# Kernel optimization log

Measured on AMD Instinct MI355X. Metric: run time of the kernel, lower is better.

Reference implementation:

```python
import jax, jax.numpy as jnp
import numpy as np

B, C, H, W = 8, 80, 128, 128
K = 100
MAX_OBJS = 128
N_GT = 256  # 32 GT boxes per image
HM_W, WH_W, OFF_W = 1.0, 0.1, 1.0
BETA = 0.1  # iou_map weight ('Ct IoU Loss x 0.1')


def setup_inputs() -> dict:
    key = jax.random.key(0)
    ks = jax.random.split(key, 12)
    hm = jax.random.normal(ks[0], (B, C, H, W), jnp.float32)
    wh = jax.random.normal(ks[1], (B, 2, H, W), jnp.float32) * 2.0 + 8.0
    reg = jax.random.normal(ks[2], (B, 2, H, W), jnp.float32) * 0.1
    hm_target = jax.random.uniform(ks[3], (B, C, H, W), jnp.float32) * 0.99
    wh_target = jax.random.uniform(ks[4], (B, MAX_OBJS, 2), jnp.float32) * 20.0 + 2.0
    reg_target = jax.random.uniform(ks[5], (B, MAX_OBJS, 2), jnp.float32)
    reg_mask = jax.random.randint(ks[6], (B, MAX_OBJS), 0, 2).astype(jnp.int32)
    ind = jax.random.randint(ks[7], (B, MAX_OBJS), 0, H * W).astype(jnp.int32)
    cx = jax.random.uniform(ks[8], (N_GT,)) * (W - 1)
    cy = jax.random.uniform(ks[9], (N_GT,)) * (H - 1)
    bw = jax.random.uniform(ks[10], (N_GT,)) * 30.0 + 2.0
    bh = jax.random.uniform(ks[11], (N_GT,)) * 30.0 + 2.0
    target_box = jnp.stack([cx - bw / 2, cy - bh / 2, cx + bw / 2, cy + bh / 2], -1).astype(jnp.float32)
    target_bidx = jnp.repeat(jnp.arange(B), N_GT // B).astype(jnp.int32)
    return {"hm": hm, "wh": wh, "reg": reg, "hm_target": hm_target,
            "wh_target": wh_target, "reg_target": reg_target,
            "reg_mask": reg_mask, "ind": ind,
            "target_box": target_box, "target_bidx": target_bidx}


def _gather_feat(feat, ind):
    # feat [B, ch, H, W], ind [B, M] spatial indices -> [B, M, ch]
    b, ch = feat.shape[0], feat.shape[1]
    f = feat.reshape(b, ch, -1).transpose(0, 2, 1)  # [B, HW, ch]
    return jnp.take_along_axis(f, ind[:, :, None], axis=1)


def _pairwise_iou(boxes1, boxes2):
    # boxes1 [K,4], boxes2 [N,4], xyxy -> [K,N]
    a1 = jnp.maximum(boxes1[:, 2] - boxes1[:, 0], 0.0) * jnp.maximum(boxes1[:, 3] - boxes1[:, 1], 0.0)
    a2 = jnp.maximum(boxes2[:, 2] - boxes2[:, 0], 0.0) * jnp.maximum(boxes2[:, 3] - boxes2[:, 1], 0.0)
    lt = jnp.maximum(boxes1[:, None, :2], boxes2[None, :, :2])
    rb = jnp.minimum(boxes1[:, None, 2:], boxes2[None, :, 2:])
    whi = jnp.clip(rb - lt, 0.0)
    inter = whi[..., 0] * whi[..., 1]
    union = a1[:, None] + a2[None, :] - inter
    return inter / jnp.maximum(union, 1e-7)


def _decode(hm_s, wh, reg):
    # _nms: 3x3 max-pool peak keeping
    hmax = jax.lax.reduce_window(hm_s, -jnp.inf, jax.lax.max,
                                 (1, 1, 3, 3), (1, 1, 1, 1),
                                 [(0, 0), (0, 0), (1, 1), (1, 1)])
    hm_k = jnp.where(hmax == hm_s, hm_s, 0.0)
    # global top-K over C*H*W (equivalent to per-class topK then topK-of-topK)
    scores, inds = jax.lax.top_k(hm_k.reshape(B, -1), K)
    clses = inds // (H * W)
    sinds = inds % (H * W)
    ys_i = sinds // W
    xs_i = sinds % W
    r = _gather_feat(reg, sinds)  # [B,K,2] sub-pixel offsets
    xs = xs_i.astype(jnp.float32) + r[..., 0]
    ys = ys_i.astype(jnp.float32) + r[..., 1]
    w = _gather_feat(wh, sinds)   # [B,K,2]
    boxes = jnp.stack([xs - w[..., 0] / 2, ys - w[..., 1] / 2,
                       xs + w[..., 0] / 2, ys + w[..., 1] / 2], -1)
    return boxes, scores, clses, ys_i, xs_i


def _focal_loss(pred, gt):
    # CenterNet focal loss; pred already sigmoid+clamped
    pos = gt == 1.0
    neg_w = (1.0 - gt) ** 4
    pos_loss = jnp.sum(jnp.where(pos, jnp.log(pred) * (1.0 - pred) ** 2, 0.0))
    neg_loss = jnp.sum(jnp.where(pos, 0.0, jnp.log(1.0 - pred) * pred ** 2 * neg_w))
    num_pos = jnp.sum(pos.astype(jnp.float32))
    return jnp.where(num_pos > 0, -(pos_loss + neg_loss) / jnp.maximum(num_pos, 1.0), -neg_loss)


def _reg_l1(out, mask, ind, tgt):
    pred = _gather_feat(out, ind)                       # [B, M, 2]
    m = jnp.broadcast_to(mask.astype(jnp.float32)[:, :, None], pred.shape)
    return jnp.sum(jnp.abs(pred * m - tgt * m)) / (jnp.sum(m) + 1e-4)


def reference(hm, wh, reg, hm_target, wh_target, reg_target, reg_mask, ind, target_box, target_bidx):
    hm_s = jnp.clip(jax.nn.sigmoid(hm), 1e-4, 1.0 - 1e-4)  # _sigmoid
    boxes, scores, clses, ys_i, xs_i = _decode(hm_s, wh, reg)
    # per-image pairwise IoU vs GT boxes of the same image, max over GT
    iou_all = jax.vmap(lambda bx: _pairwise_iou(bx, target_box))(boxes)  # [B,K,N]
    bmask = target_bidx[None, None, :] == jnp.arange(B)[:, None, None]
    iou = jnp.max(jnp.where(bmask, iou_all, 0.0), axis=-1)              # [B,K]
    # scatter IoU into dense heatmap-shaped iou_map at (b, cls, y, x)
    b_idx = jnp.broadcast_to(jnp.arange(B)[:, None], (B, K))
    iou_map = jnp.zeros_like(hm_s).at[b_idx, clses, ys_i, xs_i].set(iou)
    hm_t = jnp.clip(hm_target + BETA * iou_map, 0.0, 1.0)
    hm_loss = _focal_loss(hm_s, hm_t)
    wh_loss = _reg_l1(wh, reg_mask, ind, wh_target)
    off_loss = _reg_l1(reg, reg_mask, ind, reg_target)
    loss = HM_W * hm_loss + WH_W * wh_loss + OFF_W * off_loss
    return loss, hm_loss, wh_loss, off_loss
```

## Files before the change

kernel.cpp:

```cpp
#include <hip/hip_runtime.h>
#include <math.h>

#define B_ 8
#define C_ 80
#define H_ 128
#define W_ 128
#define K_ 100
#define MAXOBJS_ 128
#define NGT_ 256
#define HW_ (H_*W_)
#define CHW_ (C_*H_*W_)
#define TOT_ (B_*CHW_)
#define NBINS_ 4096
#define BCAP_ 4096
#define DCAP_ 128
#define CAPLDS_ 3072
#define DLOC_ 128
#define BLOC_ 768
#define NEGINF_ (-INFINITY)

#define OFF_LISTCNT 96
#define OFF_HIST   128
#define OFF_THR    131200
#define OFF_CNTA   131264
#define OFF_CNTB   131296
#define OFF_DEFV   131328
#define OFF_DEFI   135424
#define OFF_BORV   139520
#define OFF_BORI   270592
#define OFF_LIST   401664
#define ZERO_BYTES 131328
#define CAP_REQ    196608ull
#define CAP_MAX    262144ull

__device__ __forceinline__ unsigned skey(float x){
    unsigned u = __float_as_uint(x);
    return (u & 0x80000000u) ? ~u : (u | 0x80000000u);
}

__device__ __forceinline__ void find_thr(const unsigned* __restrict__ lh,
                                         unsigned* __restrict__ part,
                                         unsigned target,
                                         unsigned* out_thr, unsigned* out_cum){
    int t = threadIdx.x;
    unsigned s = 0;
    #pragma unroll
    for(int k=0;k<16;++k) s += lh[t*16+k];
    part[t] = s;
    __syncthreads();
    for(int off=1; off<256; off<<=1){
        unsigned v = (t+off<256) ? part[t+off] : 0u;
        __syncthreads();
        part[t] += v;
        __syncthreads();
    }
    unsigned nxt = (t<255) ? part[t+1] : 0u;
    if(part[t] >= target && nxt < target){
        unsigned cum = nxt;
        int thr = t*16;
        for(int bin=t*16+15; bin>=t*16; --bin){
            unsigned c = lh[bin];
            if(cum + c >= target){ thr = bin; break; }
            cum += c;
        }
        *out_thr = (unsigned)thr;
        *out_cum = cum;
    }
    __syncthreads();
}

struct Row { float v[4]; float le, re; };

__device__ __forceinline__ Row loadrow(const float* __restrict__ P, int y, int xq){
    Row r;
    if(y < 0 || y >= H_){
        r.v[0]=r.v[1]=r.v[2]=r.v[3]=r.le=r.re=NEGINF_;
        return r;
    }
    const float4 f = *(const float4*)(P + y*W_ + xq*4);
    r.v[0]=f.x; r.v[1]=f.y; r.v[2]=f.z; r.v[3]=f.w;
    r.le = (xq==0) ? NEGINF_ : P[y*W_ + xq*4 - 1];
    r.re = (xq==31)? NEGINF_ : P[y*W_ + xq*4 + 4];
    return r;
}

__device__ __forceinline__ void hmax4(const Row& r, float h[4]){
    h[0]=fmaxf(fmaxf(r.le,  r.v[0]), r.v[1]);
    h[1]=fmaxf(fmaxf(r.v[0],r.v[1]), r.v[2]);
    h[2]=fmaxf(fmaxf(r.v[1],r.v[2]), r.v[3]);
    h[3]=fmaxf(fmaxf(r.v[2],r.v[3]), r.re);
}

__global__ __launch_bounds__(256) void k_main(const float* __restrict__ hm,
        const float* __restrict__ hmt, unsigned* __restrict__ hist,
        double* __restrict__ accum, unsigned* __restrict__ listcnt,
        int2* __restrict__ list, int capB){
    __shared__ unsigned lh[NBINS_];
    __shared__ int2 lbuf[CAPLDS_];
    __shared__ unsigned lcnt, lbase;
    __shared__ float red[256];
    int t = threadIdx.x;
    int plane = blockIdx.x;
    int b = plane / C_;
    int cls = plane - b*C_;
    const float* P = hm  + (size_t)plane*HW_;
    const float* T = hmt + (size_t)plane*HW_;
    int idx0 = cls*HW_;

    for(int i=t;i<NBINS_;i+=256) lh[i]=0u;
    if(t==0) lcnt=0u;
    __syncthreads();

    int xq = t & 31;
    int y0 = (t >> 5) * 16;
    Row rp = loadrow(P, y0-1, xq);
    Row rc = loadrow(P, y0,   xq);
    float hp[4], hc[4];
    hmax4(rp, hp); hmax4(rc, hc);
    float acc = 0.f;
    for(int rr=0; rr<16; ++rr){
        int y = y0 + rr;
        Row rn = loadrow(P, y+1, xq);
        float hn[4]; hmax4(rn, hn);
        float lr[4];
        lr[0]=fmaxf(rc.le,  rc.v[1]);
        lr[1]=fmaxf(rc.v[0],rc.v[2]);
        lr[2]=fmaxf(rc.v[1],rc.v[3]);
        lr[3]=fmaxf(rc.v[2],rc.re);
        float4 tg = *(const float4*)(T + y*W_ + xq*4);
        float tgv[4] = {tg.x, tg.y, tg.z, tg.w};
        #pragma unroll
        for(int j=0;j<4;++j){
            float v = rc.v[j];
            bool pk = (v>=lr[j]) && (v>=hp[j]) && (v>=hn[j]);
            if(pk){
                atomicAdd(&lh[skey(v)>>20], 1u);
                if(capB){
                    unsigned p = atomicAdd(&lcnt, 1u);
                    int2 e; e.x = __float_as_int(v); e.y = idx0 + y*W_ + xq*4 + j;
                    if(p < CAPLDS_) lbuf[p] = e;
                    else {
                        unsigned g = atomicAdd(&listcnt[b], 1u);
                        if(g < (unsigned)capB) list[(size_t)b*capB + g] = e;
                    }
                }
            }
            float pr = 1.f/(1.f + __expf(-v));
            pr = fminf(fmaxf(pr, 1e-4f), 1.f - 1e-4f);
            float q = 1.f - tgv[j]; float q2 = q*q;
            acc += __logf(1.f - pr) * pr * pr * q2 * q2;
        }
        rc = rn;
        #pragma unroll
        for(int j=0;j<4;++j){ hp[j]=hc[j]; hc[j]=hn[j]; }
    }
    __syncthreads();
    unsigned n = lcnt; if(n > CAPLDS_) n = CAPLDS_;
    if(capB && t==0) lbase = atomicAdd(&listcnt[b], n);
    for(int i=t;i<NBINS_;i+=256){ unsigned c=lh[i]; if(c) atomicAdd(&hist[b*NBINS_+i], c); }
    red[t] = acc;
    __syncthreads();
    if(capB){
        for(unsigned i=t;i<n;i+=256){
            unsigned g = lbase + i;
            if(g < (unsigned)capB) list[(size_t)b*capB + g] = lbuf[i];
        }
    }
    for(int s=128;s>0;s>>=1){
        if(t<s) red[t]+=red[t+s];
        __syncthreads();
    }
    if(t==0) atomicAdd(&accum[0], (double)red[0]);
}

__global__ __launch_bounds__(256) void k_scan(const int2* __restrict__ list,
        const unsigned* __restrict__ listcnt, int capB,
        const unsigned* __restrict__ hist,
        unsigned* __restrict__ cntA, unsigned* __restrict__ cntB,
        float* __restrict__ defv, int* __restrict__ defi,
        float* __restrict__ borv, int* __restrict__ bori){
    __shared__ unsigned lh[NBINS_];
    __shared__ unsigned part[256];
    __shared__ unsigned thrs, cums;
    __shared__ int2 dloc[DLOC_];
    __shared__ int2 bloc[BLOC_];
    __shared__ unsigned dc, bc, dbase, bbase;
    int b = blockIdx.x >> 6;
    int chunk = blockIdx.x & 63;
    int t = threadIdx.x;
    for(int i=t;i<NBINS_;i+=256) lh[i]=hist[b*NBINS_+i];
    if(t==0){ dc=0u; bc=0u; thrs=0u; cums=0u; }
    __syncthreads();
    find_thr(lh, part, (unsigned)K_, &thrs, &cums);
    unsigned thr = thrs;
    unsigned n = listcnt[b]; if(n > (unsigned)capB) n = (unsigned)capB;
    for(unsigned i = chunk*256u + t; i < n; i += 64u*256u){
        int2 e = list[(size_t)b*capB + i];
        float v = __int_as_float(e.x);
        unsigned bin = skey(v) >> 20;
        if(bin > thr){
            unsigned p = atomicAdd(&dc, 1u);
            if(p < DLOC_) dloc[p] = e;
            else { unsigned g = atomicAdd(&cntA[b],1u); if(g<DCAP_){ defv[b*DCAP_+g]=v; defi[b*DCAP_+g]=e.y; } }
        } else if(bin == thr){
            unsigned p = atomicAdd(&bc, 1u);
            if(p < BLOC_) bloc[p] = e;
            else { unsigned g = atomicAdd(&cntB[b],1u); if(g<BCAP_){ borv[b*BCAP_+g]=v; bori[b*BCAP_+g]=e.y; } }
        }
    }
    __syncthreads();
    unsigned dn = dc < DLOC_ ? dc : DLOC_;
    unsigned bn = bc < BLOC_ ? bc : BLOC_;
    if(t==0){
        dbase = dn ? atomicAdd(&cntA[b], dn) : 0u;
        bbase = bn ? atomicAdd(&cntB[b], bn) : 0u;
    }
    __syncthreads();
    for(unsigned i=t;i<dn;i+=256){
        unsigned g = dbase + i;
        if(g < DCAP_){ defv[b*DCAP_+g]=__int_as_float(dloc[i].x); defi[b*DCAP_+g]=dloc[i].y; }
    }
    for(unsigned i=t;i<bn;i+=256){
        unsigned g = bbase + i;
        if(g < BCAP_){ borv[b*BCAP_+g]=__int_as_float(bloc[i].x); bori[b*BCAP_+g]=bloc[i].y; }
    }
}

__global__ void k_thresh(const unsigned* __restrict__ hist, unsigned* __restrict__ thrbin){
    __shared__ unsigned lh[NBINS_];
    __shared__ unsigned part[256];
    __shared__ unsigned thrs, cums;
    int b = blockIdx.x, t = threadIdx.x;
    for(int i=t;i<NBINS_;i+=256) lh[i]=hist[b*NBINS_+i];
    if(t==0){ thrs=0u; cums=0u; }
    __syncthreads();
    find_thr(lh, part, (unsigned)K_, &thrs, &cums);
    if(t==0) thrbin[b]=thrs;
}

__device__ __forceinline__ bool is_peak_scalar(const float* __restrict__ hm, int idx, float v){
    int w = idx & (W_-1);
    int h = (idx >> 7) & (H_-1);
    bool peak = true;
    #pragma unroll
    for(int dy=-1; dy<=1; ++dy){
        int hh = h + dy;
        if(hh < 0 || hh >= H_) continue;
        #pragma unroll
        for(int dx=-1; dx<=1; ++dx){
            if(dy==0 && dx==0) continue;
            int ww = w + dx;
            if(ww < 0 || ww >= W_) continue;
            peak = peak && (v >= __ldg(&hm[idx + dy*W_ + dx]));
        }
    }
    return peak;
}

__global__ __launch_bounds__(256) void k_collect(const float* __restrict__ hm,
        const unsigned* __restrict__ thrbin,
        unsigned* __restrict__ cntA, unsigned* __restrict__ cntB,
        float* __restrict__ defv, int* __restrict__ defi,
        float* __restrict__ borv, int* __restrict__ bori){
    int idx = blockIdx.x*256 + threadIdx.x;
    float v = hm[idx];
    if(!is_peak_scalar(hm, idx, v)) return;
    int b = idx / CHW_;
    unsigned bin = skey(v) >> 20;
    unsigned thr = thrbin[b];
    if(bin > thr){
        unsigned p = atomicAdd(&cntA[b], 1u);
        if(p < DCAP_){ defv[b*DCAP_+p] = v; defi[b*DCAP_+p] = idx - b*CHW_; }
    } else if(bin == thr){
        unsigned p = atomicAdd(&cntB[b], 1u);
        if(p < BCAP_){ borv[b*BCAP_+p] = v; bori[b*BCAP_+p] = idx - b*CHW_; }
    }
}

__global__ __launch_bounds__(256) void k_select(const float* __restrict__ hm,
        const float* __restrict__ hmt, const float* __restrict__ wh,
        const float* __restrict__ reg, const float* __restrict__ tbox,
        const int* __restrict__ tbid,
        const unsigned* __restrict__ cntA, const unsigned* __restrict__ cntB,
        const float* __restrict__ defv, const int* __restrict__ defi,
        const float* __restrict__ borv, const int* __restrict__ bori,
        double* __restrict__ accum, int* __restrict__ misc){
    int b = blockIdx.x, t = threadIdx.x;
    __shared__ float sbox[NGT_][4];
    __shared__ int   sbid[NGT_];
    __shared__ float sv[BCAP_];
    __shared__ int   si[BCAP_];
    __shared__ unsigned h2[NBINS_];
    __shared__ unsigned t4[BCAP_];
    __shared__ unsigned part[256];
    __shared__ int  rvI[256];
    __shared__ int  sel[K_];
    __shared__ unsigned selc, t3c, t4c;
    __shared__ unsigned thr2s, cum2s, thr3s, need3s;
    __shared__ int wsel;

    int nA = (int)cntA[b]; if(nA>DCAP_) nA=DCAP_; if(nA>K_) nA=K_;
    int nB = (int)cntB[b]; if(nB>BCAP_) nB=BCAP_;
    int m = K_ - nA; if(m>nB) m=nB; if(m<0) m=0;

    for(int i=t;i<NGT_;i+=256){
        sbox[i][0]=tbox[i*4+0]; sbox[i][1]=tbox[i*4+1];
        sbox[i][2]=tbox[i*4+2]; sbox[i][3]=tbox[i*4+3];
        sbid[i]=tbid[i];
    }
    for(int i=t;i<nB;i+=256){ sv[i]=borv[b*BCAP_+i]; si[i]=bori[b*BCAP_+i]; }
    for(int i=t;i<nA;i+=256) sel[i]=defi[b*DCAP_+i];
    if(t==0){ selc=(unsigned)nA; t3c=0u; t4c=0u; thr2s=0u; cum2s=0u; thr3s=0u; need3s=0u; }
    for(int i=t;i<NBINS_;i+=256) h2[i]=0u;
    __syncthreads();

    if(m>0){
        for(int i=t;i<nB;i+=256) atomicAdd(&h2[(skey(sv[i])>>8)&0xFFFu], 1u);
        __syncthreads();
        find_thr(h2, part, (unsigned)m, &thr2s, &cum2s);
        unsigned thr2 = thr2s, need2 = (unsigned)m - cum2s;
        for(int i=t;i<nB;i+=256){
            unsigned sb=(skey(sv[i])>>8)&0xFFFu;
            if(sb>thr2){ unsigned p=atomicAdd(&selc,1u); if(p<K_) sel[p]=si[i]; }
            else if(sb==thr2){ unsigned p=atomicAdd(&t3c,1u); if(p<BCAP_) t4[p]=(unsigned)i; }
        }
        __syncthreads();
        unsigned nt3=t3c; if(nt3>BCAP_) nt3=BCAP_;
        part[t]=0u;
        __syncthreads();
        for(unsigned i=t;i<nt3;i+=256) atomicAdd(&part[skey(sv[t4[i]])&0xFFu], 1u);
        __syncthreads();
        for(int off=1; off<256; off<<=1){
            unsigned v = (t+off<256)? part[t+off] : 0u;
            __syncthreads();
            part[t] += v;
            __syncthreads();
        }
        {
            unsigned nxt = (t<255)? part[t+1] : 0u;
            if(part[t] >= need2 && nxt < need2){ thr3s=(unsigned)t; need3s=need2-nxt; }
        }
        __syncthreads();
        unsigned thr3=thr3s, need3=need3s;
        for(unsigned i=t;i<nt3;i+=256){
            unsigned ci=t4[i];
            unsigned lb=skey(sv[ci])&0xFFu;
            if(lb>thr3){ unsigned p=atomicAdd(&selc,1u); if(p<K_) sel[p]=si[ci]; }
            else if(lb==thr3){ unsigned p=atomicAdd(&t4c,1u); if(p<NBINS_) h2[p]=(unsigned)si[ci]; }
        }
        __syncthreads();
        unsigned n4=t4c; if(n4>NBINS_) n4=NBINS_;
        if(need3 >= n4){
            for(unsigned i=t;i<n4;i+=256){ unsigned p=atomicAdd(&selc,1u); if(p<K_) sel[p]=(int)h2[i]; }
            __syncthreads();
        } else {
            for(unsigned it=0; it<need3; ++it){
                int bi=0x7FFFFFFF;
                for(unsigned i=t;i<n4;i+=256){ int w=(int)h2[i]; bi = (w<bi)?w:bi; }
                rvI[t]=bi;
                __syncthreads();
                for(int st=128;st>0;st>>=1){
                    if(t<st){ int w=rvI[t+st]; if(w<rvI[t]) rvI[t]=w; }
                    __syncthreads();
                }
                if(t==0){ wsel=rvI[0]; unsigned p=selc; selc=p+1u; if(p<K_) sel[p]=wsel; }
                __syncthreads();
                int w=wsel;
                for(unsigned i=t;i<n4;i+=256) if((int)h2[i]==w) h2[i]=0x7FFFFFFFu;
                __syncthreads();
            }
        }
    }
    __syncthreads();

    int nsel=(int)selc; if(nsel>K_) nsel=K_;
    for(int k=t;k<nsel;k+=256){
        int idx = sel[k];
        int cls = idx / HW_;
        int sp  = idx - cls*HW_;
        int yi  = sp >> 7;
        int xi  = sp & (W_-1);
        float r0 = reg[(b*2+0)*HW_ + sp];
        float r1 = reg[(b*2+1)*HW_ + sp];
        float w0 = wh[(b*2+0)*HW_ + sp];
        float w1 = wh[(b*2+1)*HW_ + sp];
        float xs = (float)xi + r0;
        float ys = (float)yi + r1;
        float x1 = xs - w0*0.5f, y1 = ys - w1*0.5f;
        float x2 = xs + w0*0.5f, y2 = ys + w1*0.5f;
        float a1 = fmaxf(x2-x1, 0.f) * fmaxf(y2-y1, 0.f);
        float best = 0.f;
        for(int g=0; g<NGT_; ++g){
            if(sbid[g] != b) continue;
            float gx1=sbox[g][0], gy1=sbox[g][1], gx2=sbox[g][2], gy2=sbox[g][3];
            float a2 = fmaxf(gx2-gx1, 0.f) * fmaxf(gy2-gy1, 0.f);
            float ix1 = fmaxf(x1,gx1), iy1 = fmaxf(y1,gy1);
            float ix2 = fminf(x2,gx2), iy2 = fminf(y2,gy2);
            float iw = fmaxf(ix2-ix1, 0.f), ih = fmaxf(iy2-iy1, 0.f);
            float inter = iw*ih;
            float uni = a1 + a2 - inter;
            float iou = inter / fmaxf(uni, 1e-7f);
            best = fmaxf(best, iou);
        }
        int gidx = b*CHW_ + idx;
        float v = hm[gidx];
        float p = 1.f/(1.f + __expf(-v));
        p = fminf(fmaxf(p, 1e-4f), 1.f - 1e-4f);
        float gt0 = hmt[gidx];
        float q0 = 1.f - gt0; float q02 = q0*q0;
        float neg0 = __logf(1.f - p) * p * p * q02 * q02;
        float gt1 = fminf(gt0 + 0.1f*best, 1.f);
        if(gt1 == 1.f){
            atomicAdd(&misc[0], 1);
            float op = 1.f - p;
            atomicAdd(&accum[1], (double)(__logf(p)*op*op));
            atomicAdd(&accum[2], (double)(-neg0));
        } else {
            float q1 = 1.f - gt1; float q12 = q1*q1;
            float neg1 = __logf(1.f - p) * p * p * q12 * q12;
            atomicAdd(&accum[2], (double)(neg1 - neg0));
        }
    }
}

__global__ void k_regfinal(const float* __restrict__ wh, const float* __restrict__ reg,
        const float* __restrict__ wht, const float* __restrict__ regt,
        const int* __restrict__ mask, const int* __restrict__ ind,
        const double* __restrict__ accum, const int* __restrict__ misc,
        float* __restrict__ out){
    int tid = threadIdx.x;
    float whn = 0.f, offn = 0.f, ms = 0.f;
    for(int i=tid; i<B_*MAXOBJS_; i+=256){
        int b = i / MAXOBJS_;
        float mk = (float)mask[i];
        int id = ind[i];
        float p0 = wh[(b*2+0)*HW_ + id], p1 = wh[(b*2+1)*HW_ + id];
        whn += mk*(fabsf(p0 - wht[2*i]) + fabsf(p1 - wht[2*i+1]));
        float q0 = reg[(b*2+0)*HW_ + id], q1 = reg[(b*2+1)*HW_ + id];
        offn += mk*(fabsf(q0 - regt[2*i]) + fabsf(q1 - regt[2*i+1]));
        ms += 2.f*mk;
    }
    __shared__ float r0[256], r1[256], r2[256];
    r0[tid]=whn; r1[tid]=offn; r2[tid]=ms;
    __syncthreads();
    for(int st=128; st>0; st>>=1){
        if(tid<st){ r0[tid]+=r0[tid+st]; r1[tid]+=r1[tid+st]; r2[tid]+=r2[tid+st]; }
        __syncthreads();
    }
    if(tid==0){
        double neg = accum[0] + accum[2];
        double pos = accum[1];
        int np = misc[0];
        float hm_loss;
        if(np > 0) hm_loss = (float)(-(pos + neg) / (double)(np < 1 ? 1 : np));
        else       hm_loss = (float)(-neg);
        float msum = r2[0];
        float wh_loss  = r0[0] / (msum + 1e-4f);
        float off_loss = r1[0] / (msum + 1e-4f);
        float loss = hm_loss + 0.1f*wh_loss + off_loss;
        out[0]=loss; out[1]=hm_loss; out[2]=wh_loss; out[3]=off_loss;
    }
}

extern "C" void kernel_launch(void* const* d_in, const int* in_sizes, int n_in,
                              void* d_out, int out_size, void* d_ws, size_t ws_size,
                              hipStream_t stream){
    const float* hm   = (const float*)d_in[0];
    const float* wh   = (const float*)d_in[1];
    const float* reg  = (const float*)d_in[2];
    const float* hmt  = (const float*)d_in[3];
    const float* wht  = (const float*)d_in[4];
    const float* regt = (const float*)d_in[5];
    const int*   mask = (const int*)d_in[6];
    const int*   ind  = (const int*)d_in[7];
    const float* tbox = (const float*)d_in[8];
    const int*   tbid = (const int*)d_in[9];

    char* ws = (char*)d_ws;
    double*   accum   = (double*)ws;
    int*      misc    = (int*)(ws + 64);
    unsigned* listcnt = (unsigned*)(ws + OFF_LISTCNT);
    unsigned* hist    = (unsigned*)(ws + OFF_HIST);
    unsigned* thrbin  = (unsigned*)(ws + OFF_THR);
    unsigned* cntA    = (unsigned*)(ws + OFF_CNTA);
    unsigned* cntB    = (unsigned*)(ws + OFF_CNTB);
    float*    defv    = (float*)(ws + OFF_DEFV);
    int*      defi    = (int*)(ws + OFF_DEFI);
    float*    borv    = (float*)(ws + OFF_BORV);
    int*      bori    = (int*)(ws + OFF_BORI);
    int2*     list    = (int2*)(ws + OFF_LIST);

    size_t capB = 0;
    if(ws_size >= (size_t)OFF_LIST + CAP_REQ*(size_t)B_*8ull){
        capB = (ws_size - (size_t)OFF_LIST) / ((size_t)B_*8ull);
        if(capB > CAP_MAX) capB = CAP_MAX;
    }

    hipMemsetAsync(ws, 0, ZERO_BYTES, stream);
    k_main<<<B_*C_, 256, 0, stream>>>(hm, hmt, hist, accum, listcnt, list, (int)capB);
    if(capB){
        k_scan<<<B_*64, 256, 0, stream>>>(list, listcnt, (int)capB, hist,
                                          cntA, cntB, defv, defi, borv, bori);
    } else {
        k_thresh<<<B_, 256, 0, stream>>>(hist, thrbin);
        k_collect<<<TOT_/256, 256, 0, stream>>>(hm, thrbin, cntA, cntB,
                                                defv, defi, borv, bori);
    }
    k_select<<<B_, 256, 0, stream>>>(hm, hmt, wh, reg, tbox, tbid, cntA, cntB,
                                     defv, defi, borv, bori, accum, misc);
    k_regfinal<<<1, 256, 0, stream>>>(wh, reg, wht, regt, mask, ind, accum, misc,
                                      (float*)d_out);
    (void)in_sizes; (void)n_in; (void)out_size;
}
```

Baseline: 95.97 us.

## Split heatmap planes across two blocks, aggregate list appends per wavefront, hoist threshold

```diff
diff --git a/kernel.cpp b/kernel.cpp
--- a/kernel.cpp
+++ b/kernel.cpp
@@ -14,7 +14,7 @@
 #define NBINS_ 4096
 #define BCAP_ 4096
 #define DCAP_ 128
-#define CAPLDS_ 3072
+#define CAPLDS_ 1536
 #define DLOC_ 128
 #define BLOC_ 768
 #define NEGINF_ (-INFINITY)
@@ -100,25 +100,27 @@
     __shared__ unsigned lcnt, lbase;
     __shared__ float red[256];
     int t = threadIdx.x;
-    int plane = blockIdx.x;
+    int plane = blockIdx.x >> 1;
+    int half  = blockIdx.x & 1;
     int b = plane / C_;
     int cls = plane - b*C_;
     const float* P = hm  + (size_t)plane*HW_;
     const float* T = hmt + (size_t)plane*HW_;
     int idx0 = cls*HW_;
+    unsigned lane = (unsigned)(t & 63);
 
     for(int i=t;i<NBINS_;i+=256) lh[i]=0u;
     if(t==0) lcnt=0u;
     __syncthreads();
 
     int xq = t & 31;
-    int y0 = (t >> 5) * 16;
+    int y0 = half*64 + (t >> 5) * 8;
     Row rp = loadrow(P, y0-1, xq);
     Row rc = loadrow(P, y0,   xq);
     float hp[4], hc[4];
     hmax4(rp, hp); hmax4(rc, hc);
     float acc = 0.f;
-    for(int rr=0; rr<16; ++rr){
+    for(int rr=0; rr<8; ++rr){
         int y = y0 + rr;
         Row rn = loadrow(P, y+1, xq);
         float hn[4]; hmax4(rn, hn);
@@ -133,10 +135,18 @@
         for(int j=0;j<4;++j){
             float v = rc.v[j];
             bool pk = (v>=lr[j]) && (v>=hp[j]) && (v>=hn[j]);
-            if(pk){
-                atomicAdd(&lh[skey(v)>>20], 1u);
-                if(capB){
-                    unsigned p = atomicAdd(&lcnt, 1u);
+            if(pk) atomicAdd(&lh[skey(v)>>20], 1u);
+            if(capB){
+                unsigned long long mask = __ballot(pk);
+                int cnt = __popcll(mask);
+                unsigned pre = (unsigned)__popcll(mask & ((1ull<<lane)-1ull));
+                int base = 0;
+                if(cnt){
+                    if(lane==0) base = (int)atomicAdd(&lcnt, (unsigned)cnt);
+                    base = __shfl(base, 0, 64);
+                }
+                if(pk){
+                    unsigned p = (unsigned)base + pre;
                     int2 e; e.x = __float_as_int(v); e.y = idx0 + y*W_ + xq*4 + j;
                     if(p < CAPLDS_) lbuf[p] = e;
                     else {
@@ -173,26 +183,33 @@
     if(t==0) atomicAdd(&accum[0], (double)red[0]);
 }
 
+__global__ void k_thresh(const unsigned* __restrict__ hist, unsigned* __restrict__ thrbin){
+    __shared__ unsigned lh[NBINS_];
+    __shared__ unsigned part[256];
+    __shared__ unsigned thrs, cums;
+    int b = blockIdx.x, t = threadIdx.x;
+    for(int i=t;i<NBINS_;i+=256) lh[i]=hist[b*NBINS_+i];
+    if(t==0){ thrs=0u; cums=0u; }
+    __syncthreads();
+    find_thr(lh, part, (unsigned)K_, &thrs, &cums);
+    if(t==0) thrbin[b]=thrs;
+}
+
 __global__ __launch_bounds__(256) void k_scan(const int2* __restrict__ list,
         const unsigned* __restrict__ listcnt, int capB,
-        const unsigned* __restrict__ hist,
+        const unsigned* __restrict__ thrbin,
         unsigned* __restrict__ cntA, unsigned* __restrict__ cntB,
         float* __restrict__ defv, int* __restrict__ defi,
         float* __restrict__ borv, int* __restrict__ bori){
-    __shared__ unsigned lh[NBINS_];
-    __shared__ unsigned part[256];
-    __shared__ unsigned thrs, cums;
     __shared__ int2 dloc[DLOC_];
     __shared__ int2 bloc[BLOC_];
     __shared__ unsigned dc, bc, dbase, bbase;
     int b = blockIdx.x >> 6;
     int chunk = blockIdx.x & 63;
     int t = threadIdx.x;
-    for(int i=t;i<NBINS_;i+=256) lh[i]=hist[b*NBINS_+i];
-    if(t==0){ dc=0u; bc=0u; thrs=0u; cums=0u; }
-    __syncthreads();
-    find_thr(lh, part, (unsigned)K_, &thrs, &cums);
-    unsigned thr = thrs;
+    if(t==0){ dc=0u; bc=0u; }
+    __syncthreads();
+    unsigned thr = thrbin[b];
     unsigned n = listcnt[b]; if(n > (unsigned)capB) n = (unsigned)capB;
     for(unsigned i = chunk*256u + t; i < n; i += 64u*256u){
         int2 e = list[(size_t)b*capB + i];
@@ -224,18 +241,6 @@
         unsigned g = bbase + i;
         if(g < BCAP_){ borv[b*BCAP_+g]=__int_as_float(bloc[i].x); bori[b*BCAP_+g]=bloc[i].y; }
     }
-}
-
-__global__ void k_thresh(const unsigned* __restrict__ hist, unsigned* __restrict__ thrbin){
-    __shared__ unsigned lh[NBINS_];
-    __shared__ unsigned part[256];
-    __shared__ unsigned thrs, cums;
-    int b = blockIdx.x, t = threadIdx.x;
-    for(int i=t;i<NBINS_;i+=256) lh[i]=hist[b*NBINS_+i];
-    if(t==0){ thrs=0u; cums=0u; }
-    __syncthreads();
-    find_thr(lh, part, (unsigned)K_, &thrs, &cums);
-    if(t==0) thrbin[b]=thrs;
 }
 
 __device__ __forceinline__ bool is_peak_scalar(const float* __restrict__ hm, int idx, float v){
@@ -497,12 +502,12 @@
     }
 
     hipMemsetAsync(ws, 0, ZERO_BYTES, stream);
-    k_main<<<B_*C_, 256, 0, stream>>>(hm, hmt, hist, accum, listcnt, list, (int)capB);
+    k_main<<<B_*C_*2, 256, 0, stream>>>(hm, hmt, hist, accum, listcnt, list, (int)capB);
+    k_thresh<<<B_, 256, 0, stream>>>(hist, thrbin);
     if(capB){
-        k_scan<<<B_*64, 256, 0, stream>>>(list, listcnt, (int)capB, hist,
+        k_scan<<<B_*64, 256, 0, stream>>>(list, listcnt, (int)capB, thrbin,
                                           cntA, cntB, defv, defi, borv, bori);
     } else {
-        k_thresh<<<B_, 256, 0, stream>>>(hist, thrbin);
         k_collect<<<TOT_/256, 256, 0, stream>>>(hm, thrbin, cntA, cntB,
                                                 defv, defi, borv, bori);
     }
```

Result: slower. 98.93 us (+3.1%).
